# Kernel tuning notes

Measured on AMD Instinct MI355X. Metric: run time of the kernel, lower is better.

## Reference

```python
import jax, jax.numpy as jnp
import numpy as np

B = 4
C = 256
NUM_LEVELS = 5
REFINE_LEVEL = 2
NUM_POINTS = 9
GRAD_MUL = 0.1
SIZES = [160, 80, 40, 20, 10]


def conv2d(x, w, b=None, pad=0):
    out = jax.lax.conv_general_dilated(
        x, w, (1, 1), [(pad, pad), (pad, pad)],
        dimension_numbers=("NCHW", "OIHW", "NCHW"))
    if b is not None:
        out = out + b[None, :, None, None]
    return out


def nearest_resize(x, oh, ow):
    # torch F.interpolate(mode='nearest'): src index = floor(dst * in/out)
    H, W = x.shape[-2], x.shape[-1]
    iy = (jnp.arange(oh) * H) // oh
    ix = (jnp.arange(ow) * W) // ow
    return jnp.take(jnp.take(x, iy, axis=-2), ix, axis=-1)


def max_pool_to(x, oh, ow):
    # adaptive_max_pool2d with exactly-divisible sizes == strided max pool
    b, c, H, W = x.shape
    kh, kw = H // oh, W // ow
    return x.reshape(b, c, oh, kh, ow, kw).max(axis=(3, 5))


def deform_conv(x, offset, weight):
    # DeformConv v1 (mmcv), stride 1, pad 1, 3x3 kernel, no bias.
    # offset channels interleaved (dy, dx) per kernel point.
    b, c, H, W = x.shape
    K = weight.shape[-2] * weight.shape[-1]  # 9
    dy = offset[:, 0::2]  # (B,K,H,W)
    dx = offset[:, 1::2]
    base = jnp.arange(-1, 2, dtype=x.dtype)
    base_y = jnp.repeat(base, 3)  # (9,)
    base_x = jnp.tile(base, 3)
    py = jnp.arange(H, dtype=x.dtype)[None, None, :, None] + base_y[None, :, None, None] + dy
    px = jnp.arange(W, dtype=x.dtype)[None, None, None, :] + base_x[None, :, None, None] + dx
    y0 = jnp.floor(py)
    x0 = jnp.floor(px)
    xf = x.reshape(b, c, H * W)

    def gather(iy, ix):
        valid = ((iy >= 0) & (iy <= H - 1) & (ix >= 0) & (ix <= W - 1)).astype(x.dtype)
        flat = (jnp.clip(iy, 0, H - 1).astype(jnp.int32) * W
                + jnp.clip(ix, 0, W - 1).astype(jnp.int32)).reshape(b, -1)
        g = jax.vmap(lambda xb, ib: jnp.take(xb, ib, axis=1))(xf, flat)
        return g.reshape(b, c, K, H, W) * valid[:, None]

    wy1 = py - y0
    wx1 = px - x0
    wy0 = 1.0 - wy1
    wx0 = 1.0 - wx1
    val = (gather(y0, x0) * (wy0 * wx0)[:, None]
           + gather(y0, x0 + 1.0) * (wy0 * wx1)[:, None]
           + gather(y0 + 1.0, x0) * (wy1 * wx0)[:, None]
           + gather(y0 + 1.0, x0 + 1.0) * (wy1 * wx1)[:, None])  # (B,C,K,H,W)
    return jnp.einsum("bckhw,ock->bohw", val, weight.reshape(weight.shape[0], c, K))


def setup_inputs() -> dict:
    key = jax.random.key(0)
    ks = jax.random.split(key, 12)
    inp = {}
    for i, s in enumerate(SIZES):
        inp[f"x{i}"] = jax.random.normal(ks[i], (B, C, s, s), jnp.float32)
    inp["w_red1"] = jax.random.normal(ks[5], (NUM_LEVELS, 1, C, 3, 3), jnp.float32) * 0.02
    inp["b_red1"] = jnp.zeros((NUM_LEVELS, 1), jnp.float32)
    inp["w_red2"] = jax.random.normal(ks[6], (NUM_LEVELS, 1, C, 3, 3), jnp.float32) * 0.02
    inp["b_red2"] = jnp.zeros((NUM_LEVELS, 1), jnp.float32)
    inp["w_pts_conv"] = jax.random.normal(ks[7], (C, C, 3, 3), jnp.float32) * 0.02
    inp["b_pts_conv"] = jnp.zeros((C,), jnp.float32)
    inp["w_pts_out"] = jax.random.normal(ks[8], (2 * NUM_POINTS, C, 1, 1), jnp.float32) * 0.01
    inp["b_pts_out"] = jnp.zeros((2 * NUM_POINTS,), jnp.float32)
    inp["w_refine"] = jax.random.normal(ks[9], (C, C, 3, 3), jnp.float32) * 0.01
    return inp


def reference(x0, x1, x2, x3, x4, w_red1, b_red1, w_red2, b_red2,
              w_pts_conv, b_pts_conv, w_pts_out, b_pts_out, w_refine):
    inputs = [x0, x1, x2, x3, x4]
    gh, gw = inputs[REFINE_LEVEL].shape[-2], inputs[REFINE_LEVEL].shape[-1]
    feats = [max_pool_to(xi, gh, gw) if i < REFINE_LEVEL else nearest_resize(xi, gh, gw)
             for i, xi in enumerate(inputs)]
    ori_fe = sum(feats) / len(feats)

    pts = conv2d(jax.nn.relu(conv2d(ori_fe, w_pts_conv, b_pts_conv, pad=1)),
                 w_pts_out, b_pts_out, pad=0)
    pts_gm = (1.0 - GRAD_MUL) * jax.lax.stop_gradient(pts) + GRAD_MUL * pts

    base = jnp.arange(-1, 2, dtype=jnp.float32)
    base_off = jnp.stack([jnp.repeat(base, 3), jnp.tile(base, 3)], axis=1).reshape(-1)
    dcn_offset = pts_gm - base_off[None, :, None, None]

    bsf = jax.nn.relu(deform_conv(ori_fe, dcn_offset, w_refine))

    outs = []
    for i, xi in enumerate(inputs):
        h, w = xi.shape[-2], xi.shape[-1]
        # ConvModule default: conv -> (no norm) -> ReLU; then tanh per forward
        basic = jnp.tanh(jax.nn.relu(conv2d(xi, w_red1[i], b_red1[i], pad=1)))
        com = jnp.tanh(jax.nn.relu(conv2d(xi, w_red2[i], b_red2[i], pad=1)))
        att = nearest_resize(bsf, h, w) * (basic + com)
        outs.append(xi + att)
    return tuple(outs)
```

## Files before the change

### kernel.cpp

```cpp
#include <hip/hip_runtime.h>
#include <hip/hip_bf16.h>
#include <math.h>

constexpr int B_ = 4;
constexpr int C_ = 256;
constexpr int GH = 40, GW = 40, GP = 1600;
constexpr int KDIM = C_ * 9;
constexpr int MT = B_ * GP;

typedef __attribute__((ext_vector_type(8))) short short8b;
typedef __attribute__((ext_vector_type(4))) float f32x4;

__device__ inline ushort f2b(float f) {
    __hip_bfloat16 h = __float2bfloat16(f);
    return *reinterpret_cast<ushort*>(&h);
}
__device__ inline float b2f(ushort u) {
    unsigned v = (unsigned)u << 16;
    return *reinterpret_cast<float*>(&v);
}

__global__ __launch_bounds__(256) void fe_kernel(const float* __restrict__ x0,
                                                 const float* __restrict__ x1,
                                                 const float* __restrict__ x2,
                                                 const float* __restrict__ x3,
                                                 const float* __restrict__ x4,
                                                 float* __restrict__ fe_pm) {
    __shared__ float tile[64][65];
    int pix0 = blockIdx.x * 64;
    int c0 = blockIdx.y * 64;
    int b = blockIdx.z;
    int lx = threadIdx.x & 63;
    int ly = threadIdx.x >> 6;

    int pix = pix0 + lx;
    int h = pix / GW, w = pix - (pix / GW) * GW;
#pragma unroll
    for (int r = 0; r < 64; r += 4) {
        int c = c0 + ly + r;
        size_t bc = (size_t)b * C_ + c;
        const float* p0 = x0 + bc * 25600;
        float m0 = -INFINITY;
#pragma unroll
        for (int dy = 0; dy < 4; ++dy)
#pragma unroll
            for (int dx = 0; dx < 4; ++dx)
                m0 = fmaxf(m0, p0[(4 * h + dy) * 160 + 4 * w + dx]);
        const float* p1 = x1 + bc * 6400;
        float m1 = -INFINITY;
#pragma unroll
        for (int dy = 0; dy < 2; ++dy)
#pragma unroll
            for (int dx = 0; dx < 2; ++dx)
                m1 = fmaxf(m1, p1[(2 * h + dy) * 80 + 2 * w + dx]);
        float v2 = x2[bc * GP + pix];
        float v3 = x3[bc * 400 + (h / 2) * 20 + (w / 2)];
        float v4 = x4[bc * 100 + (h / 4) * 10 + (w / 4)];
        tile[ly + r][lx] = (m0 + m1 + v2 + v3 + v4) * 0.2f;
    }
    __syncthreads();
#pragma unroll
    for (int r = 0; r < 64; r += 4) {
        int p = ly + r;
        fe_pm[((size_t)b * GP + pix0 + p) * C_ + c0 + lx] = tile[lx][p];
    }
}

__global__ void wcvt_kernel(const float* __restrict__ wA, const float* __restrict__ wB,
                            ushort* __restrict__ oA, ushort* __restrict__ oB) {
    const float* w = blockIdx.y ? wB : wA;
    ushort* out = blockIdx.y ? oB : oA;
    int idx = blockIdx.x * 256 + threadIdx.x;
    int o = idx / KDIM;
    int rem = idx - o * KDIM;
    int c = rem / 9, t = rem - c * 9;
    out[(size_t)o * KDIM + t * 256 + c] = f2b(w[idx]);
}

template <int MODE>
__global__ __launch_bounds__(256) void mfma_gemm(const float* __restrict__ fe_pm,
                                                 const float* __restrict__ pts,
                                                 const ushort* __restrict__ Bw,
                                                 const float* __restrict__ bias,
                                                 float* __restrict__ Cout) {
    __shared__ ushort As[64 * 64];
    __shared__ ushort Bs[64 * 64];
    int tid = threadIdx.x;
    int lane = tid & 63;
    int wid = tid >> 6;
    int wm = wid >> 1, wn = wid & 1;
    int m0 = blockIdx.x * 64;
    int n0 = blockIdx.y * 64;
    int b = m0 / GP;
    int pix0 = m0 - b * GP;

    int rw = tid >> 2;
    int q = tid & 3;
    int so0 = ((2 * q) ^ (rw & 7)) * 8;
    int so1 = ((2 * q + 1) ^ (rw & 7)) * 8;

    int pix = pix0 + rw;
    int h = pix / GW, w = pix - (pix / GW) * GW;
    const float* fb = fe_pm + (size_t)b * GP * C_;
    const float* pb = pts + (size_t)b * 18 * GP + pix;

    f32x4 acc[2][2];
#pragma unroll
    for (int i = 0; i < 2; ++i)
#pragma unroll
        for (int j = 0; j < 2; ++j) acc[i][j] = (f32x4){0.f, 0.f, 0.f, 0.f};

    short8b pa0, pa1, pb0, pb1;

    auto stageA = [&](int k0, short8b& a0, short8b& a1) {
        int t = k0 >> 8;
        int c0 = (k0 & 255) + q * 16;
        float v[16];
        if (MODE == 0) {
            int dy = t / 3 - 1, dx = t - (t / 3) * 3 - 1;
            int yy = h + dy, xx = w + dx;
            if (yy >= 0 && yy < GH && xx >= 0 && xx < GW) {
                const float4* src = (const float4*)(fb + (size_t)(yy * GW + xx) * C_ + c0);
#pragma unroll
                for (int j = 0; j < 4; ++j) {
                    float4 f4 = src[j];
                    v[4 * j] = f4.x; v[4 * j + 1] = f4.y; v[4 * j + 2] = f4.z; v[4 * j + 3] = f4.w;
                }
            } else {
#pragma unroll
                for (int j = 0; j < 16; ++j) v[j] = 0.f;
            }
        } else {
            float py = (float)h + pb[(2 * t) * GP];
            float px = (float)w + pb[(2 * t + 1) * GP];
            float y0f = floorf(py), x0f = floorf(px);
            int y0 = (int)y0f, x0i = (int)x0f;
            float wy1 = py - y0f, wx1 = px - x0f;
            float wy0 = 1.f - wy1, wx0 = 1.f - wx1;
            float wt[4] = {wy0 * wx0, wy0 * wx1, wy1 * wx0, wy1 * wx1};
            int ty[4] = {y0, y0, y0 + 1, y0 + 1};
            int tx[4] = {x0i, x0i + 1, x0i, x0i + 1};
#pragma unroll
            for (int j = 0; j < 16; ++j) v[j] = 0.f;
#pragma unroll
            for (int tp = 0; tp < 4; ++tp) {
                if (ty[tp] >= 0 && ty[tp] < GH && tx[tp] >= 0 && tx[tp] < GW) {
                    const float4* src =
                        (const float4*)(fb + (size_t)(ty[tp] * GW + tx[tp]) * C_ + c0);
#pragma unroll
                    for (int j = 0; j < 4; ++j) {
                        float4 f4 = src[j];
                        v[4 * j] += wt[tp] * f4.x;
                        v[4 * j + 1] += wt[tp] * f4.y;
                        v[4 * j + 2] += wt[tp] * f4.z;
                        v[4 * j + 3] += wt[tp] * f4.w;
                    }
                }
            }
        }
#pragma unroll
        for (int j = 0; j < 8; ++j) a0[j] = (short)f2b(v[j]);
#pragma unroll
        for (int j = 0; j < 8; ++j) a1[j] = (short)f2b(v[8 + j]);
    };
    auto stageB = [&](int k0, short8b& b0, short8b& b1) {
        const ushort* src = Bw + (size_t)(n0 + rw) * KDIM + k0 + q * 16;
        b0 = *(const short8b*)src;
        b1 = *(const short8b*)(src + 8);
    };

    stageA(0, pa0, pa1);
    stageB(0, pb0, pb1);

    for (int k0 = 0; k0 < KDIM; k0 += 64) {
        __syncthreads();
        *(short8b*)(As + rw * 64 + so0) = pa0;
        *(short8b*)(As + rw * 64 + so1) = pa1;
        *(short8b*)(Bs + rw * 64 + so0) = pb0;
        *(short8b*)(Bs + rw * 64 + so1) = pb1;
        __syncthreads();
        if (k0 + 64 < KDIM) {
            stageA(k0 + 64, pa0, pa1);
            stageB(k0 + 64, pb0, pb1);
        }
#pragma unroll
        for (int kq = 0; kq < 2; ++kq) {
            int k16 = kq * 4 + (lane >> 4);
            short8b af[2], bfr[2];
#pragma unroll
            for (int i = 0; i < 2; ++i) {
                int rA = wm * 32 + i * 16 + (lane & 15);
                af[i] = *(const short8b*)(As + rA * 64 + ((k16 ^ (rA & 7)) * 8));
                int rB = wn * 32 + i * 16 + (lane & 15);
                bfr[i] = *(const short8b*)(Bs + rB * 64 + ((k16 ^ (rB & 7)) * 8));
            }
#pragma unroll
            for (int in = 0; in < 2; ++in)
#pragma unroll
                for (int im = 0; im < 2; ++im)
                    acc[in][im] = __builtin_amdgcn_mfma_f32_16x16x32_bf16(
                        bfr[in], af[im], acc[in][im], 0, 0, 0);
        }
    }

    float* Cb = Cout + (size_t)b * C_ * GP;
#pragma unroll
    for (int in = 0; in < 2; ++in) {
#pragma unroll
        for (int r = 0; r < 4; ++r) {
            int n = n0 + wn * 32 + in * 16 + (lane >> 4) * 4 + r;
            float bv = bias ? bias[n] : 0.f;
#pragma unroll
            for (int im = 0; im < 2; ++im) {
                int m = pix0 + wm * 32 + im * 16 + (lane & 15);
                Cb[(size_t)n * GP + m] = fmaxf(acc[in][im][r] + bv, 0.f);
            }
        }
    }
}

__global__ void pts_kernel(const float* __restrict__ p1, const float* __restrict__ wpo,
                           const float* __restrict__ bpo, float* __restrict__ pts) {
    int idx = blockIdx.x * 256 + threadIdx.x;
    int pix = idx % GP;
    int p = (idx / GP) % 18;
    int b = idx / (GP * 18);
    const float* pb = p1 + (size_t)b * C_ * GP + pix;
    const float* wp = wpo + p * C_;
    float s = bpo[p];
    for (int c = 0; c < C_; ++c) s += pb[(size_t)c * GP] * wp[c];
    pts[idx] = s;
}

__device__ constexpr int L_S[5] = {160, 80, 40, 20, 10};
__device__ constexpr int L_NPX[5] = {102400, 25600, 6400, 1600, 400};
__device__ constexpr int YK_START[5] = {0, 400, 500, 525, 532};
__device__ constexpr int FC_START[5] = {0, 1600, 2000, 2100, 2125};
__device__ constexpr size_t L_YBASE[5] = {0, 7372800, 9216000, 9676800, 9792000};
__device__ constexpr size_t L_OUT[5] = {0, 26214400, 32768000, 34406400, 34816000};

__device__ inline int lvl_of(int bx, const int* start) {
    return (bx >= start[4]) ? 4 : (bx >= start[3]) ? 3 : (bx >= start[2]) ? 2
           : (bx >= start[1]) ? 1 : 0;
}

__global__ __launch_bounds__(256) void yk_all(const float* __restrict__ x0,
                                              const float* __restrict__ x1,
                                              const float* __restrict__ x2,
                                              const float* __restrict__ x3,
                                              const float* __restrict__ x4,
                                              const float* __restrict__ w_red1,
                                              const float* __restrict__ w_red2,
                                              ushort* __restrict__ y_all) {
    int bx = blockIdx.x;
    int lvl = lvl_of(bx, YK_START);
    const float* x = lvl == 0 ? x0 : lvl == 1 ? x1 : lvl == 2 ? x2 : lvl == 3 ? x3 : x4;
    int s = L_S[lvl];
    int npx = L_NPX[lvl];
    int bp = (bx - YK_START[lvl]) * 256 + threadIdx.x;
    int g = blockIdx.y;
    if (bp >= npx) return;
    int ss_ = s * s;
    int b = bp / ss_;
    int p = bp - b * ss_;
    const float* xg = x + ((size_t)b * C_ + g * 64) * ss_ + p;
    const float* w1g = w_red1 + (size_t)lvl * KDIM + g * 64 * 9;
    const float* w2g = w_red2 + (size_t)lvl * KDIM + g * 64 * 9;
    float a1[9] = {}, a2[9] = {};
#pragma unroll 4
    for (int ci = 0; ci < 64; ++ci) {
        float v = xg[(size_t)ci * ss_];
#pragma unroll
        for (int t = 0; t < 9; ++t) {
            a1[t] += w1g[ci * 9 + t] * v;
            a2[t] += w2g[ci * 9 + t] * v;
        }
    }
    ushort* yb = y_all + L_YBASE[lvl] + bp;
#pragma unroll
    for (int t = 0; t < 9; ++t) {
        yb[(size_t)(g * 18 + t) * npx] = f2b(a1[t]);
        yb[(size_t)(g * 18 + 9 + t) * npx] = f2b(a2[t]);
    }
}

__global__ __launch_bounds__(256) void fincomb_all(const float* __restrict__ x0,
                                                   const float* __restrict__ x1,
                                                   const float* __restrict__ x2,
                                                   const float* __restrict__ x3,
                                                   const float* __restrict__ x4,
                                                   const ushort* __restrict__ y_all,
                                                   const float* __restrict__ b_red1,
                                                   const float* __restrict__ b_red2,
                                                   const float* __restrict__ bsf,
                                                   float* __restrict__ out) {
    __shared__ float red[2][4][64];
    __shared__ float amap_s[64];
    int bx = blockIdx.x;
    int lvl = lvl_of(bx, FC_START);
    const float* x = lvl == 0 ? x0 : lvl == 1 ? x1 : lvl == 2 ? x2 : lvl == 3 ? x3 : x4;
    int s = L_S[lvl];
    int npx = L_NPX[lvl];
    const ushort* y = y_all + L_YBASE[lvl];
    float* out_l = out + L_OUT[lvl];
    int lane = threadIdx.x & 63;
    int grp = threadIdx.x >> 6;
    int pix_g = (bx - FC_START[lvl]) * 64 + lane;
    bool valid = pix_g < npx;
    int pg = valid ? pix_g : 0;
    int ss_ = s * s;
    int b = pg / ss_;
    int pix = pg - b * ss_;
    int h = pix / s, w = pix - h * s;
    const ushort* yg = y + (size_t)grp * 18 * npx;
    float s1 = 0.f, s2 = 0.f;
#pragma unroll
    for (int t = 0; t < 9; ++t) {
        int dy = t / 3 - 1, dx = t % 3 - 1;
        int hy = h + dy, wx = w + dx;
        if (hy >= 0 && hy < s && wx >= 0 && wx < s) {
            int qq = pg + dy * s + dx;
            s1 += b2f(yg[(size_t)t * npx + qq]);
            s2 += b2f(yg[(size_t)(9 + t) * npx + qq]);
        }
    }
    red[0][grp][lane] = s1;
    red[1][grp][lane] = s2;
    __syncthreads();
    if (grp == 0) {
        float t1 = red[0][0][lane] + red[0][1][lane] + red[0][2][lane] + red[0][3][lane];
        float t2 = red[1][0][lane] + red[1][1][lane] + red[1][2][lane] + red[1][3][lane];
        t1 = tanhf(fmaxf(t1 + b_red1[lvl], 0.f));
        t2 = tanhf(fmaxf(t2 + b_red2[lvl], 0.f));
        amap_s[lane] = t1 + t2;
    }
    __syncthreads();
    if (!valid) return;
    float av = amap_s[lane];
    int gh = h * GH / s, gw = w * GW / s;
    const float* bb = bsf + (size_t)b * C_ * GP + gh * GW + gw;
    const float* xp = x + ((size_t)b * C_ + grp * 64) * ss_ + pix;
    float* op = out_l + ((size_t)b * C_ + grp * 64) * ss_ + pix;
#pragma unroll 4
    for (int ci = 0; ci < 64; ++ci) {
        int c = grp * 64 + ci;
        op[(size_t)ci * ss_] = xp[(size_t)ci * ss_] + bb[(size_t)c * GP] * av;
    }
}

extern "C" void kernel_launch(void* const* d_in, const int* in_sizes, int n_in,
                              void* d_out, int out_size, void* d_ws, size_t ws_size,
                              hipStream_t stream) {
    const float* x[5];
    for (int i = 0; i < 5; ++i) x[i] = (const float*)d_in[i];
    const float* w_red1 = (const float*)d_in[5];
    const float* b_red1 = (const float*)d_in[6];
    const float* w_red2 = (const float*)d_in[7];
    const float* b_red2 = (const float*)d_in[8];
    const float* w_pts_conv = (const float*)d_in[9];
    const float* b_pts_conv = (const float*)d_in[10];
    const float* w_pts_out = (const float*)d_in[11];
    const float* b_pts_out = (const float*)d_in[12];
    const float* w_refine = (const float*)d_in[13];
    float* out = (float*)d_out;

    float* ws = (float*)d_ws;
    float* fe_pm = ws;
    float* p1 = fe_pm + 1638400;
    float* pts = p1 + 1638400;
    float* bsf = pts + 115200;
    ushort* y_all = (ushort*)(bsf + 1638400);
    ushort* Wb1 = y_all + 9820800;
    ushort* Wb2 = Wb1 + (size_t)C_ * KDIM;

    fe_kernel<<<dim3(25, 4, B_), 256, 0, stream>>>(x[0], x[1], x[2], x[3], x[4], fe_pm);
    wcvt_kernel<<<dim3(2304, 2), 256, 0, stream>>>(w_pts_conv, w_refine, Wb1, Wb2);
    mfma_gemm<0><<<dim3(100, 4), 256, 0, stream>>>(fe_pm, nullptr, Wb1, b_pts_conv, p1);
    pts_kernel<<<450, 256, 0, stream>>>(p1, w_pts_out, b_pts_out, pts);
    mfma_gemm<1><<<dim3(100, 4), 256, 0, stream>>>(fe_pm, pts, Wb2, nullptr, bsf);
    yk_all<<<dim3(534, 4), 256, 0, stream>>>(x[0], x[1], x[2], x[3], x[4],
                                             w_red1, w_red2, y_all);
    fincomb_all<<<2132, 256, 0, stream>>>(x[0], x[1], x[2], x[3], x[4], y_all,
                                          b_red1, b_red2, bsf, out);
}
```

Measured before the change: 280.7 us.

## Split-K the two conv GEMMs three ways and double-buffer LDS tiles

```diff
diff --git a/kernel.cpp b/kernel.cpp
--- a/kernel.cpp
+++ b/kernel.cpp
@@ -6,7 +6,8 @@
 constexpr int C_ = 256;
 constexpr int GH = 40, GW = 40, GP = 1600;
 constexpr int KDIM = C_ * 9;
-constexpr int MT = B_ * GP;
+constexpr int KSPL = 768;
+constexpr int NELEM = B_ * C_ * GP;
 
 typedef __attribute__((ext_vector_type(8))) short short8b;
 typedef __attribute__((ext_vector_type(4))) float f32x4;
@@ -81,16 +82,16 @@
 __global__ __launch_bounds__(256) void mfma_gemm(const float* __restrict__ fe_pm,
                                                  const float* __restrict__ pts,
                                                  const ushort* __restrict__ Bw,
-                                                 const float* __restrict__ bias,
-                                                 float* __restrict__ Cout) {
-    __shared__ ushort As[64 * 64];
-    __shared__ ushort Bs[64 * 64];
+                                                 float* __restrict__ Cpart) {
+    __shared__ ushort As[2][64 * 64];
+    __shared__ ushort Bs[2][64 * 64];
     int tid = threadIdx.x;
     int lane = tid & 63;
     int wid = tid >> 6;
     int wm = wid >> 1, wn = wid & 1;
     int m0 = blockIdx.x * 64;
     int n0 = blockIdx.y * 64;
+    int zs = blockIdx.z;
     int b = m0 / GP;
     int pix0 = m0 - b * GP;
 
@@ -110,10 +111,10 @@
 #pragma unroll
         for (int j = 0; j < 2; ++j) acc[i][j] = (f32x4){0.f, 0.f, 0.f, 0.f};
 
-    short8b pa0, pa1, pb0, pb1;
+    short8b pa0, pa1, pbv0, pbv1;
 
     auto stageA = [&](int k0, short8b& a0, short8b& a1) {
-        int t = k0 >> 8;
+        int t = zs * 3 + (k0 >> 8);
         int c0 = (k0 & 255) + q * 16;
         float v[16];
         if (MODE == 0) {
@@ -164,24 +165,28 @@
         for (int j = 0; j < 8; ++j) a1[j] = (short)f2b(v[8 + j]);
     };
     auto stageB = [&](int k0, short8b& b0, short8b& b1) {
-        const ushort* src = Bw + (size_t)(n0 + rw) * KDIM + k0 + q * 16;
+        const ushort* src = Bw + (size_t)(n0 + rw) * KDIM + zs * KSPL + k0 + q * 16;
         b0 = *(const short8b*)src;
         b1 = *(const short8b*)(src + 8);
     };
+    auto lds_write = [&](int buf, short8b a0, short8b a1, short8b b0, short8b b1) {
+        *(short8b*)(As[buf] + rw * 64 + so0) = a0;
+        *(short8b*)(As[buf] + rw * 64 + so1) = a1;
+        *(short8b*)(Bs[buf] + rw * 64 + so0) = b0;
+        *(short8b*)(Bs[buf] + rw * 64 + so1) = b1;
+    };
 
     stageA(0, pa0, pa1);
-    stageB(0, pb0, pb1);
-
-    for (int k0 = 0; k0 < KDIM; k0 += 64) {
-        __syncthreads();
-        *(short8b*)(As + rw * 64 + so0) = pa0;
-        *(short8b*)(As + rw * 64 + so1) = pa1;
-        *(short8b*)(Bs + rw * 64 + so0) = pb0;
-        *(short8b*)(Bs + rw * 64 + so1) = pb1;
-        __syncthreads();
-        if (k0 + 64 < KDIM) {
-            stageA(k0 + 64, pa0, pa1);
-            stageB(k0 + 64, pb0, pb1);
+    stageB(0, pbv0, pbv1);
+    lds_write(0, pa0, pa1, pbv0, pbv1);
+    __syncthreads();
+
+    constexpr int NCH = KSPL / 64;
+    for (int kc = 0; kc < NCH; ++kc) {
+        int cur = kc & 1;
+        if (kc + 1 < NCH) {
+            stageA((kc + 1) * 64, pa0, pa1);
+            stageB((kc + 1) * 64, pbv0, pbv1);
         }
 #pragma unroll
         for (int kq = 0; kq < 2; ++kq) {
@@ -190,9 +195,9 @@
 #pragma unroll
             for (int i = 0; i < 2; ++i) {
                 int rA = wm * 32 + i * 16 + (lane & 15);
-                af[i] = *(const short8b*)(As + rA * 64 + ((k16 ^ (rA & 7)) * 8));
+                af[i] = *(const short8b*)(As[cur] + rA * 64 + ((k16 ^ (rA & 7)) * 8));
                 int rB = wn * 32 + i * 16 + (lane & 15);
-                bfr[i] = *(const short8b*)(Bs + rB * 64 + ((k16 ^ (rB & 7)) * 8));
+                bfr[i] = *(const short8b*)(Bs[cur] + rB * 64 + ((k16 ^ (rB & 7)) * 8));
             }
 #pragma unroll
             for (int in = 0; in < 2; ++in)
@@ -201,22 +206,32 @@
                     acc[in][im] = __builtin_amdgcn_mfma_f32_16x16x32_bf16(
                         bfr[in], af[im], acc[in][im], 0, 0, 0);
         }
-    }
-
-    float* Cb = Cout + (size_t)b * C_ * GP;
+        if (kc + 1 < NCH) lds_write(cur ^ 1, pa0, pa1, pbv0, pbv1);
+        __syncthreads();
+    }
+
+    float* Cb = Cpart + (size_t)zs * NELEM + (size_t)b * C_ * GP;
 #pragma unroll
     for (int in = 0; in < 2; ++in) {
 #pragma unroll
         for (int r = 0; r < 4; ++r) {
             int n = n0 + wn * 32 + in * 16 + (lane >> 4) * 4 + r;
-            float bv = bias ? bias[n] : 0.f;
 #pragma unroll
             for (int im = 0; im < 2; ++im) {
                 int m = pix0 + wm * 32 + im * 16 + (lane & 15);
-                Cb[(size_t)n * GP + m] = fmaxf(acc[in][im][r] + bv, 0.f);
+                Cb[(size_t)n * GP + m] = acc[in][im][r];
             }
         }
     }
+}
+
+__global__ __launch_bounds__(256) void reduce3_kernel(const float* __restrict__ parts,
+                                                      const float* __restrict__ bias,
+                                                      float* __restrict__ dst) {
+    int idx = blockIdx.x * 256 + threadIdx.x;
+    float v = parts[idx] + parts[idx + NELEM] + parts[idx + 2 * NELEM];
+    if (bias) v += bias[(idx / GP) & 255];
+    dst[idx] = fmaxf(v, 0.f);
 }
 
 __global__ void pts_kernel(const float* __restrict__ p1, const float* __restrict__ wpo,
@@ -369,15 +384,18 @@
     float* p1 = fe_pm + 1638400;
     float* pts = p1 + 1638400;
     float* bsf = pts + 115200;
-    ushort* y_all = (ushort*)(bsf + 1638400);
+    float* parts = bsf + 1638400;
+    ushort* y_all = (ushort*)(parts + 4915200);
     ushort* Wb1 = y_all + 9820800;
     ushort* Wb2 = Wb1 + (size_t)C_ * KDIM;
 
     fe_kernel<<<dim3(25, 4, B_), 256, 0, stream>>>(x[0], x[1], x[2], x[3], x[4], fe_pm);
     wcvt_kernel<<<dim3(2304, 2), 256, 0, stream>>>(w_pts_conv, w_refine, Wb1, Wb2);
-    mfma_gemm<0><<<dim3(100, 4), 256, 0, stream>>>(fe_pm, nullptr, Wb1, b_pts_conv, p1);
+    mfma_gemm<0><<<dim3(100, 4, 3), 256, 0, stream>>>(fe_pm, nullptr, Wb1, parts);
+    reduce3_kernel<<<6400, 256, 0, stream>>>(parts, b_pts_conv, p1);
     pts_kernel<<<450, 256, 0, stream>>>(p1, w_pts_out, b_pts_out, pts);
-    mfma_gemm<1><<<dim3(100, 4), 256, 0, stream>>>(fe_pm, pts, Wb2, nullptr, bsf);
+    mfma_gemm<1><<<dim3(100, 4, 3), 256, 0, stream>>>(fe_pm, pts, Wb2, parts);
+    reduce3_kernel<<<6400, 256, 0, stream>>>(parts, nullptr, bsf);
     yk_all<<<dim3(534, 4), 256, 0, stream>>>(x[0], x[1], x[2], x[3], x[4],
                                              w_red1, w_red2, y_all);
     fincomb_all<<<2132, 256, 0, stream>>>(x[0], x[1], x[2], x[3], x[4], y_all,
```

After: 279.0 us. About the same (-0.6%).
